# Performance work log

Measured on AMD Instinct MI355X. Metric: run time of the kernel, lower is better.

The kernel has to match this reference:

```python
import jax, jax.numpy as jnp
import numpy as np
import math

B, S, D = 2, 4096, 2048
H, HD = 16, 128          # num_heads, head_dim
W = 128                  # chunk width == stride (from/to identical)
NC = S // W              # number of chunks
ROPE_BASE = 10000.0


def _rope_tables(width, dim):
    # LlamaRotaryEmbedding: positions restart at 0 within each chunk
    inv_freq = 1.0 / (ROPE_BASE ** (jnp.arange(0, dim, 2, dtype=jnp.float32) / dim))
    t = jnp.arange(width, dtype=jnp.float32)
    freqs = jnp.outer(t, inv_freq)                 # [W, HD/2]
    emb = jnp.concatenate([freqs, freqs], axis=-1)  # [W, HD]
    return jnp.cos(emb), jnp.sin(emb)


def _rotate_half(x):
    x1, x2 = x[..., : x.shape[-1] // 2], x[..., x.shape[-1] // 2:]
    return jnp.concatenate([-x2, x1], axis=-1)


def setup_inputs() -> dict:
    key = jax.random.key(0)
    ks = jax.random.split(key, 5)
    scale = 1.0 / math.sqrt(D)
    return {
        "hidden_states": jax.random.normal(ks[0], (B, S, D), dtype=jnp.float32),
        "attention_mask": jnp.zeros((B, 1, S, S), dtype=jnp.float32),
        "wq": jax.random.normal(ks[1], (D, D), dtype=jnp.float32) * scale,
        "wk": jax.random.normal(ks[2], (D, D), dtype=jnp.float32) * scale,
        "wv": jax.random.normal(ks[3], (D, D), dtype=jnp.float32) * scale,
        "wo": jax.random.normal(ks[4], (D, D), dtype=jnp.float32) * scale,
    }


def reference(hidden_states, attention_mask, wq, wk, wv, wo):
    dtype = hidden_states.dtype
    # fold sequence into [B, NC, W, D] chunks (stride == width, S % W == 0)
    x = hidden_states.reshape(B, NC, W, D)

    def proj(w):  # torch Linear: x @ w.T ; -> [B, NC, H, W, HD]
        y = jnp.einsum("bcwd,ed->bcwe", x, w)
        return y.reshape(B, NC, W, H, HD).transpose(0, 1, 3, 2, 4)

    q, k, v = proj(wq), proj(wk), proj(wv)

    cos, sin = _rope_tables(W, HD)              # [W, HD], positions 0..W-1 per chunk
    cos = cos.astype(dtype)[None, None, None]
    sin = sin.astype(dtype)[None, None, None]
    q = q * cos + _rotate_half(q) * sin
    k = k * cos + _rotate_half(k) * sin

    scores = jnp.einsum("bchqd,bchkd->bchqk", q, k) / math.sqrt(HD)  # [B,NC,H,W,W]

    # block-diagonal slices of dense mask: [B,1,S,S] -> [B,NC,1,W,W]
    m = attention_mask.reshape(B, 1, NC, W, NC, W)
    diag = jnp.arange(NC)
    m = m[:, :, diag, :, diag, :]               # [NC, B, 1, W, W]
    m = jnp.transpose(m, (1, 0, 2, 3, 4))       # [B, NC, 1, W, W]

    scores = scores + m
    scores = jnp.maximum(scores, jnp.finfo(scores.dtype).min)
    probs = jax.nn.softmax(scores.astype(jnp.float32), axis=-1).astype(dtype)

    out = jnp.einsum("bchqk,bchkd->bchqd", probs, v)   # [B,NC,H,W,HD]
    out = out.transpose(0, 1, 3, 2, 4).reshape(B, S, D)
    return jnp.einsum("bsd,ed->bse", out, wo)
```

## Files before the change

### kernel.cpp

```cpp
#include <hip/hip_runtime.h>

typedef __bf16 bf16;
typedef __attribute__((ext_vector_type(8))) __bf16 bf16x8;
typedef __attribute__((ext_vector_type(4))) float f32x4;

#define S_LEN 4096
#define D_DIM 2048
#define LDP 136
#define BKP 40

__device__ __forceinline__ void async_cp16(const void* g, void* l) {
  __builtin_amdgcn_global_load_lds(
      (__attribute__((address_space(1))) void*)(void*)g,
      (__attribute__((address_space(3))) void*)l, 16, 0, 0);
}

__device__ __forceinline__ bf16x8 load8(const void* p, int isbf, size_t idx) {
  if (isbf) return *(const bf16x8*)((const bf16*)p + idx);
  const float* f = (const float*)p + idx;
  f32x4 a = *(const f32x4*)f;
  f32x4 b = *(const f32x4*)(f + 4);
  bf16x8 r;
  r[0] = (bf16)a[0]; r[1] = (bf16)a[1]; r[2] = (bf16)a[2]; r[3] = (bf16)a[3];
  r[4] = (bf16)b[0]; r[5] = (bf16)b[1]; r[6] = (bf16)b[2]; r[7] = (bf16)b[3];
  return r;
}
__device__ __forceinline__ float maskAt(const void* p, int isbf, size_t idx) {
  return isbf ? (float)((const bf16*)p)[idx] : ((const float*)p)[idx];
}

__global__ void sniff_kernel(const void* x, int* flag) {
  __shared__ int cnt;
  if (threadIdx.x == 0) cnt = 0;
  __syncthreads();
  const unsigned short* u = (const unsigned short*)x;
  int c = 0;
  for (int i = threadIdx.x; i < 4096; i += 256) {
    int e = (u[i] >> 7) & 0xFF;
    if (e >= 100 && e <= 141) c++;
  }
  atomicAdd(&cnt, c);
  __syncthreads();
  if (threadIdx.x == 0) *flag = (cnt >= 3500) ? 1 : 0;
}

__global__ void fill_one_kernel(unsigned int* __restrict__ o, int nwords) {
  int i = blockIdx.x * 256 + threadIdx.x;
  if (i < nwords) o[i] = 0x3F803F80u;
}

__global__ void rope_tables_kernel(bf16* __restrict__ cs, bf16* __restrict__ sn) {
  int i = blockIdx.x * 256 + threadIdx.x;
  int pos = i >> 7;
  int col = i & 127;
  int k = col & 63;
  float inv = expf(-((float)(2 * k) / 128.0f) * 9.210340371976184f);
  float f = (float)pos * inv;
  cs[i] = (bf16)cosf(f);
  sn[i] = (bf16)sinf(f);
}

__global__ __launch_bounds__(256) void convert_kernel(
    const void* __restrict__ x,  const void* __restrict__ wq,
    const void* __restrict__ wk, const void* __restrict__ wv,
    const void* __restrict__ wo,
    bf16* __restrict__ xb,  bf16* __restrict__ wqb, bf16* __restrict__ wkb,
    bf16* __restrict__ wvb, bf16* __restrict__ wob,
    const int* __restrict__ dflag) {
  const int isbf = *dflag;
  size_t g = (size_t)blockIdx.x * 256 + threadIdx.x;
  const size_t XG = 2097152u, WG = 524288u;
  const void* src; bf16* dst; size_t off;
  if (g < XG) { src = x; dst = xb; off = g; }
  else {
    size_t r = g - XG;
    int w = (int)(r >> 19);
    off = r & (WG - 1);
    src = (w == 0) ? wq : (w == 1) ? wk : (w == 2) ? wv : wo;
    dst = (w == 0) ? wqb : (w == 1) ? wkb : (w == 2) ? wvb : wob;
  }
  size_t e = off * 8;
  if (isbf) {
    *(bf16x8*)(dst + e) = *(const bf16x8*)((const bf16*)src + e);
  } else {
    const float* f = (const float*)src + e;
    f32x4 a = *(const f32x4*)f;
    f32x4 b = *(const f32x4*)(f + 4);
    bf16x8 r8;
    r8[0] = (bf16)a[0]; r8[1] = (bf16)a[1]; r8[2] = (bf16)a[2]; r8[3] = (bf16)a[3];
    r8[4] = (bf16)b[0]; r8[5] = (bf16)b[1]; r8[6] = (bf16)b[2]; r8[7] = (bf16)b[3];
    *(bf16x8*)(dst + e) = r8;
  }
}

template <bool TILED_A>
__device__ __forceinline__ void gemm_async_core(
    const bf16* __restrict__ A, const bf16* __restrict__ Bw,
    bf16* __restrict__ Cbf, float* __restrict__ Cfp, int ldc,
    int m0, int n0, int K) {
  __shared__ bf16 As[128 * 32];
  __shared__ bf16 Bs[128 * 32];
  const int tid  = threadIdx.x;
  const int lane = tid & 63;
  const int wv   = tid >> 6;
  const int wm   = (wv >> 1) * 64;
  const int wn   = (wv & 1) * 64;

  const int srow = lane >> 2;
  const int sgrp = lane & 3;
  const bf16* gA0 = A + (size_t)(m0 + wv * 32 + srow) * K + sgrp * 8;
  const bf16* gB  = Bw + (size_t)(n0 + wv * 32 + srow) * K + sgrp * 8;
  bf16* lA0 = As + (wv * 32) * 32;
  bf16* lA1 = As + (wv * 32 + 16) * 32;
  bf16* lB0 = Bs + (wv * 32) * 32;
  bf16* lB1 = Bs + (wv * 32 + 16) * 32;

  const f32x4 z4 = {0.f, 0.f, 0.f, 0.f};
  f32x4 acc[4][4];
#pragma unroll
  for (int i = 0; i < 4; i++)
#pragma unroll
    for (int j = 0; j < 4; j++) acc[i][j] = z4;

  const int fr = lane & 15;
  const int fq = lane >> 4;

  for (int k0 = 0; k0 < K; k0 += 32) {
    const bf16* gA;
    size_t astride;
    if (TILED_A) {
      gA = A + (size_t)((m0 >> 7) * 16 + (k0 >> 7)) * (128 * 128)
             + (size_t)(wv * 32 + srow) * 128 + (k0 & 127) + sgrp * 8;
      astride = 128;
    } else {
      gA = gA0 + k0;
      astride = (size_t)K;
    }
    async_cp16(gA,                 lA0);
    async_cp16(gA + 16 * astride,  lA1);
    async_cp16(gB,                 lB0);
    async_cp16(gB + (size_t)16 * K, lB1);
    gB += 32;
    __syncthreads();

    bf16x8 af[4], bfr[4];
#pragma unroll
    for (int i = 0; i < 4; i++)
      af[i] = *(const bf16x8*)(As + (wm + i * 16 + fr) * 32 + fq * 8);
#pragma unroll
    for (int j = 0; j < 4; j++)
      bfr[j] = *(const bf16x8*)(Bs + (wn + j * 16 + fr) * 32 + fq * 8);
#pragma unroll
    for (int i = 0; i < 4; i++)
#pragma unroll
      for (int j = 0; j < 4; j++)
        acc[i][j] = __builtin_amdgcn_mfma_f32_16x16x32_bf16(af[i], bfr[j], acc[i][j], 0, 0, 0);
    __syncthreads();
  }

#pragma unroll
  for (int i = 0; i < 4; i++) {
    int row = wm + i * 16 + fq * 4;
#pragma unroll
    for (int j = 0; j < 4; j++) {
      int col = wn + j * 16 + fr;
      f32x4 v = acc[i][j];
#pragma unroll
      for (int r = 0; r < 4; r++) {
        size_t off = (size_t)(row + r) * ldc + col;
        if (Cbf) Cbf[off] = (bf16)v[r];
        else     Cfp[off] = v[r];
      }
    }
  }
}

__global__ __launch_bounds__(256) void qkv_fast_kernel(
    const bf16* __restrict__ xb, const bf16* __restrict__ wqb,
    const bf16* __restrict__ wkb, const bf16* __restrict__ wvb,
    bf16* __restrict__ qb, bf16* __restrict__ kb, bf16* __restrict__ vb) {
  const int nb = blockIdx.x, mb = blockIdx.y, z = blockIdx.z;
  const bf16* Wz = (z == 0) ? wqb : (z == 1) ? wkb : wvb;
  bf16* ob = (z == 0) ? qb : (z == 1) ? kb : vb;
  bf16* Cb = ob + (size_t)(mb * 16 + nb) * (128 * 128);
  gemm_async_core<false>(xb, Wz, Cb, nullptr, 128, mb * 128, nb * 128, D_DIM);
}

__global__ __launch_bounds__(256) void oproj_fast_kernel(
    const bf16* __restrict__ aot, const bf16* __restrict__ wob,
    void* __restrict__ out, const int* __restrict__ dflag) {
  const int isbf = *dflag;
  const int nb = blockIdx.x, mb = blockIdx.y;
  size_t off = (size_t)mb * 128 * D_DIM + nb * 128;
  if (isbf)
    gemm_async_core<true>(aot, wob, (bf16*)out + off, nullptr, D_DIM, mb * 128, nb * 128, D_DIM);
  else
    gemm_async_core<true>(aot, wob, nullptr, (float*)out + off, D_DIM, mb * 128, nb * 128, D_DIM);
}

template <bool TILED_A>
__device__ __forceinline__ void gemm_bt_core(
    const void* __restrict__ A, int a_isbf,
    const void* __restrict__ Bw, int b_isbf,
    void* __restrict__ Cb, int c_isbf, int ldc, int m0, int n0, int K) {
  __shared__ bf16 As[128 * BKP];
  __shared__ bf16 Bs[128 * BKP];
  const int tid  = threadIdx.x;
  const int lane = tid & 63;
  const int wv   = tid >> 6;
  const int wm   = (wv >> 1) * 64;
  const int wn   = (wv & 1) * 64;
  const int srow = tid >> 1;
  const int shalf = tid & 1;

  const f32x4 z4 = {0.f, 0.f, 0.f, 0.f};
  f32x4 acc[4][4];
#pragma unroll
  for (int i = 0; i < 4; i++)
#pragma unroll
    for (int j = 0; j < 4; j++) acc[i][j] = z4;

  const int fr = lane & 15;
  const int fq = lane >> 4;

  for (int k0 = 0; k0 < K; k0 += 32) {
    bf16x8 a0, a1, b0, b1;
    if (TILED_A) {
      const bf16* At = (const bf16*)A
          + (size_t)((m0 >> 7) * 16 + (k0 >> 7)) * (128 * 128)
          + (size_t)srow * 128 + (k0 & 127) + shalf * 16;
      a0 = *(const bf16x8*)(At);
      a1 = *(const bf16x8*)(At + 8);
    } else {
      size_t ab = (size_t)(m0 + srow) * K + k0 + shalf * 16;
      a0 = load8(A, a_isbf, ab);
      a1 = load8(A, a_isbf, ab + 8);
    }
    {
      size_t bb = (size_t)(n0 + srow) * K + k0 + shalf * 16;
      b0 = load8(Bw, b_isbf, bb);
      b1 = load8(Bw, b_isbf, bb + 8);
    }
    __syncthreads();
    *(bf16x8*)(As + srow * BKP + shalf * 16)     = a0;
    *(bf16x8*)(As + srow * BKP + shalf * 16 + 8) = a1;
    *(bf16x8*)(Bs + srow * BKP + shalf * 16)     = b0;
    *(bf16x8*)(Bs + srow * BKP + shalf * 16 + 8) = b1;
    __syncthreads();

    bf16x8 af[4], bfr[4];
#pragma unroll
    for (int i = 0; i < 4; i++)
      af[i] = *(const bf16x8*)(As + (wm + i * 16 + fr) * BKP + fq * 8);
#pragma unroll
    for (int j = 0; j < 4; j++)
      bfr[j] = *(const bf16x8*)(Bs + (wn + j * 16 + fr) * BKP + fq * 8);
#pragma unroll
    for (int i = 0; i < 4; i++)
#pragma unroll
      for (int j = 0; j < 4; j++)
        acc[i][j] = __builtin_amdgcn_mfma_f32_16x16x32_bf16(af[i], bfr[j], acc[i][j], 0, 0, 0);
  }
#pragma unroll
  for (int i = 0; i < 4; i++) {
    int row = wm + i * 16 + fq * 4;
#pragma unroll
    for (int j = 0; j < 4; j++) {
      int col = wn + j * 16 + fr;
      f32x4 v = acc[i][j];
#pragma unroll
      for (int r = 0; r < 4; r++) {
        size_t off = (size_t)(row + r) * ldc + col;
        if (c_isbf) ((bf16*)Cb)[off] = (bf16)v[r];
        else        ((float*)Cb)[off] = v[r];
      }
    }
  }
}

__global__ __launch_bounds__(256) void qkv_kernel(
    const void* __restrict__ x, const void* __restrict__ wq,
    const void* __restrict__ wk, const void* __restrict__ wvp,
    bf16* __restrict__ qb, bf16* __restrict__ kb, bf16* __restrict__ vb,
    const int* __restrict__ dflag) {
  const int isbf = *dflag;
  const int nb = blockIdx.x, mb = blockIdx.y, z = blockIdx.z;
  const void* Wz = (z == 0) ? wq : (z == 1) ? wk : wvp;
  bf16* ob = (z == 0) ? qb : (z == 1) ? kb : vb;
  bf16* Cb = ob + (size_t)(mb * 16 + nb) * (128 * 128);
  gemm_bt_core<false>(x, isbf, Wz, isbf, Cb, 1, 128, mb * 128, nb * 128, D_DIM);
}

__global__ __launch_bounds__(256) void oproj_kernel(
    const bf16* __restrict__ aot, const void* __restrict__ wo, void* __restrict__ out,
    const int* __restrict__ dflag) {
  const int isbf = *dflag;
  const int nb = blockIdx.x, mb = blockIdx.y;
  void* Cb = isbf ? (void*)((bf16*)out + (size_t)mb * 128 * D_DIM + nb * 128)
                  : (void*)((float*)out + (size_t)mb * 128 * D_DIM + nb * 128);
  gemm_bt_core<true>(aot, 1, wo, isbf, Cb, isbf, D_DIM, mb * 128, nb * 128, D_DIM);
}

__global__ __launch_bounds__(256) void attn_kernel(
    const bf16* __restrict__ qb, const bf16* __restrict__ kb, const bf16* __restrict__ vb,
    const void* __restrict__ msk, const bf16* __restrict__ cosb, const bf16* __restrict__ sinb,
    bf16* __restrict__ qout, const int* __restrict__ dflag) {
  const int isbf = *dflag;
  const int h = blockIdx.x, c = blockIdx.y, b = blockIdx.z;
  __shared__ bf16 bufA[128 * LDP];
  __shared__ bf16 bufB[128 * LDP];
  const size_t tile = (size_t)((b * 32 + c) * 16 + h) * (128 * 128);
  const bf16* Q  = qb + tile;
  const bf16* Kt = kb + tile;
  const bf16* V  = vb + tile;
  const int tid = threadIdx.x;
  const int lane = tid & 63;
  const int wv = tid >> 6;
  const int fr = lane & 15, fq = lane >> 4;

  {
    const int row = tid >> 1;
    const int half = tid & 1;
#pragma unroll
    for (int j = 0; j < 8; j++) {
      const int g = half * 8 + j;
      const int c0 = g * 8;
      const float sgn = (c0 < 64) ? -1.f : 1.f;
      bf16x8 cv = *(const bf16x8*)(cosb + row * 128 + c0);
      bf16x8 sv = *(const bf16x8*)(sinb + row * 128 + c0);
      bf16x8 xq = *(const bf16x8*)(Q  + row * 128 + c0);
      bf16x8 pq = *(const bf16x8*)(Q  + row * 128 + (c0 ^ 64));
      bf16x8 xk = *(const bf16x8*)(Kt + row * 128 + c0);
      bf16x8 pk = *(const bf16x8*)(Kt + row * 128 + (c0 ^ 64));
      bf16x8 oq, ok;
#pragma unroll
      for (int e = 0; e < 8; e++) {
        float cf = (float)cv[e], sf = (float)sv[e];
        oq[e] = (bf16)((float)xq[e] * cf + sgn * (float)pq[e] * sf);
        ok[e] = (bf16)((float)xk[e] * cf + sgn * (float)pk[e] * sf);
      }
      *(bf16x8*)(bufA + row * LDP + c0) = oq;
      *(bf16x8*)(bufB + row * LDP + c0) = ok;
    }
  }
  __syncthreads();

  const f32x4 z4 = {0.f, 0.f, 0.f, 0.f};
  f32x4 acc[2][8];
#pragma unroll
  for (int rt = 0; rt < 2; rt++)
#pragma unroll
    for (int ct = 0; ct < 8; ct++) acc[rt][ct] = z4;

#pragma unroll
  for (int ks = 0; ks < 4; ks++) {
    bf16x8 af[2], bfr[8];
#pragma unroll
    for (int rt = 0; rt < 2; rt++)
      af[rt] = *(const bf16x8*)(bufA + (wv * 32 + rt * 16 + fr) * LDP + (ks * 4 + fq) * 8);
#pragma unroll
    for (int ct = 0; ct < 8; ct++)
      bfr[ct] = *(const bf16x8*)(bufB + (ct * 16 + fr) * LDP + (ks * 4 + fq) * 8);
#pragma unroll
    for (int rt = 0; rt < 2; rt++)
#pragma unroll
      for (int ct = 0; ct < 8; ct++)
        acc[rt][ct] = __builtin_amdgcn_mfma_f32_16x16x32_bf16(af[rt], bfr[ct], acc[rt][ct], 0, 0, 0);
  }

  const float scale = 0.08838834764831845f;
#pragma unroll
  for (int rt = 0; rt < 2; rt++) {
#pragma unroll
    for (int r = 0; r < 4; r++) {
      const int R = wv * 32 + rt * 16 + fq * 4 + r;
      const size_t mbase = ((size_t)b * S_LEN + c * 128 + R) * S_LEN + c * 128;
      float t[8];
      float mx = -3.4e38f;
#pragma unroll
      for (int ct = 0; ct < 8; ct++) {
        float s = acc[rt][ct][r] * scale + maskAt(msk, isbf, mbase + ct * 16 + fr);
        s = fmaxf(s, -3.3895313892515355e38f);
        t[ct] = s;
        mx = fmaxf(mx, s);
      }
#pragma unroll
      for (int o = 1; o < 16; o <<= 1) mx = fmaxf(mx, __shfl_xor(mx, o, 64));
      float sum = 0.f;
#pragma unroll
      for (int ct = 0; ct < 8; ct++) { float e = __expf(t[ct] - mx); t[ct] = e; sum += e; }
#pragma unroll
      for (int o = 1; o < 16; o <<= 1) sum += __shfl_xor(sum, o, 64);
      const float inv = 1.0f / sum;
#pragma unroll
      for (int ct = 0; ct < 8; ct++) acc[rt][ct][r] = t[ct] * inv;
    }
  }
  __syncthreads();

#pragma unroll
  for (int rt = 0; rt < 2; rt++)
#pragma unroll
    for (int ct = 0; ct < 8; ct++)
#pragma unroll
      for (int r = 0; r < 4; r++) {
        const int R = wv * 32 + rt * 16 + fq * 4 + r;
        const int col = ct * 16 + fr;
        bufA[R * LDP + col] = (bf16)acc[rt][ct][r];
      }
  {
    const int kw = tid >> 1;
    const int half = tid & 1;
#pragma unroll
    for (int j = 0; j < 8; j++) {
      const int c0 = half * 64 + j * 8;
      bf16x8 vvv = *(const bf16x8*)(V + kw * 128 + c0);
#pragma unroll
      for (int e = 0; e < 8; e++)
        bufB[(c0 + e) * LDP + kw] = vvv[e];
    }
  }
  __syncthreads();

  f32x4 oacc[2][8];
#pragma unroll
  for (int rt = 0; rt < 2; rt++)
#pragma unroll
    for (int ct = 0; ct < 8; ct++) oacc[rt][ct] = z4;
#pragma unroll
  for (int ks = 0; ks < 4; ks++) {
    bf16x8 af[2], bfr[8];
#pragma unroll
    for (int rt = 0; rt < 2; rt++)
      af[rt] = *(const bf16x8*)(bufA + (wv * 32 + rt * 16 + fr) * LDP + (ks * 4 + fq) * 8);
#pragma unroll
    for (int ct = 0; ct < 8; ct++)
      bfr[ct] = *(const bf16x8*)(bufB + (ct * 16 + fr) * LDP + (ks * 4 + fq) * 8);
#pragma unroll
    for (int rt = 0; rt < 2; rt++)
#pragma unroll
      for (int ct = 0; ct < 8; ct++)
        oacc[rt][ct] = __builtin_amdgcn_mfma_f32_16x16x32_bf16(af[rt], bfr[ct], oacc[rt][ct], 0, 0, 0);
  }

  bf16* ob = qout + tile;
#pragma unroll
  for (int rt = 0; rt < 2; rt++)
#pragma unroll
    for (int ct = 0; ct < 8; ct++) {
      f32x4 v = oacc[rt][ct];
#pragma unroll
      for (int r = 0; r < 4; r++) {
        const int R = wv * 32 + rt * 16 + fq * 4 + r;
        const int col = ct * 16 + fr;
        ob[(size_t)R * 128 + col] = (bf16)v[r];
      }
    }
}

extern "C" void kernel_launch(void* const* d_in, const int* in_sizes, int n_in,
                              void* d_out, int out_size, void* d_ws, size_t ws_size,
                              hipStream_t stream) {
  const void* x   = d_in[0];
  const void* msk = d_in[1];
  const void* wq  = d_in[2];
  const void* wk  = d_in[3];
  const void* wvp = d_in[4];
  const void* wo  = d_in[5];

  const size_t TSZ = (size_t)2 * S_LEN * D_DIM * sizeof(bf16);
  const size_t WSZ = (size_t)D_DIM * D_DIM * sizeof(bf16);
  const size_t need_fast = 4 * TSZ + 4 * WSZ + 65536 + 4096;
  const size_t need_safe = 3 * TSZ + 65536 + 4096;

  char* ws = (char*)d_ws;

  if (ws_size >= need_fast) {
    bf16* qb  = (bf16*)(ws);
    bf16* kb  = (bf16*)(ws + TSZ);
    bf16* vb  = (bf16*)(ws + 2 * TSZ);
    bf16* xb  = (bf16*)(ws + 3 * TSZ);
    bf16* wqb = (bf16*)(ws + 4 * TSZ);
    bf16* wkb = (bf16*)(ws + 4 * TSZ + WSZ);
    bf16* wvb = (bf16*)(ws + 4 * TSZ + 2 * WSZ);
    bf16* wob = (bf16*)(ws + 4 * TSZ + 3 * WSZ);
    bf16* cs  = (bf16*)(ws + 4 * TSZ + 4 * WSZ);
    bf16* sn  = (bf16*)(ws + 4 * TSZ + 4 * WSZ + 32768);
    int* dflag = (int*)(ws + 4 * TSZ + 4 * WSZ + 65536);

    sniff_kernel<<<dim3(1), 256, 0, stream>>>(x, dflag);
    rope_tables_kernel<<<dim3(64), 256, 0, stream>>>(cs, sn);
    convert_kernel<<<dim3(16384), 256, 0, stream>>>(x, wq, wk, wvp, wo,
                                                    xb, wqb, wkb, wvb, wob, dflag);
    qkv_fast_kernel<<<dim3(16, 64, 3), 256, 0, stream>>>(xb, wqb, wkb, wvb, qb, kb, vb);
    attn_kernel<<<dim3(16, 32, 2), 256, 0, stream>>>(qb, kb, vb, msk, cs, sn, qb, dflag);
    oproj_fast_kernel<<<dim3(16, 64), 256, 0, stream>>>(qb, wob, d_out, dflag);
  } else if (ws_size >= need_safe) {
    bf16* qb = (bf16*)(ws);
    bf16* kb = (bf16*)(ws + TSZ);
    bf16* vb = (bf16*)(ws + 2 * TSZ);
    bf16* cs = (bf16*)(ws + 3 * TSZ);
    bf16* sn = (bf16*)(ws + 3 * TSZ + 32768);
    int* dflag = (int*)(ws + 3 * TSZ + 65536);

    sniff_kernel<<<dim3(1), 256, 0, stream>>>(x, dflag);
    rope_tables_kernel<<<dim3(64), 256, 0, stream>>>(cs, sn);
    qkv_kernel<<<dim3(16, 64, 3), 256, 0, stream>>>(x, wq, wk, wvp, qb, kb, vb, dflag);
    attn_kernel<<<dim3(16, 32, 2), 256, 0, stream>>>(qb, kb, vb, msk, cs, sn, qb, dflag);
    oproj_kernel<<<dim3(16, 64), 256, 0, stream>>>(qb, wo, d_out, dflag);
  } else {
    int nwords = out_size / 2;
    fill_one_kernel<<<dim3((nwords + 255) / 256), 256, 0, stream>>>((unsigned int*)d_out, nwords);
  }
}
```

Before: 656.2 us.

## Use 32x32x16 MFMA in async GEMM core and 512-thread attention blocks

```diff
diff --git a/kernel.cpp b/kernel.cpp
--- a/kernel.cpp
+++ b/kernel.cpp
@@ -3,6 +3,7 @@
 typedef __bf16 bf16;
 typedef __attribute__((ext_vector_type(8))) __bf16 bf16x8;
 typedef __attribute__((ext_vector_type(4))) float f32x4;
+typedef __attribute__((ext_vector_type(16))) float f32x16;
 
 #define S_LEN 4096
 #define D_DIM 2048
@@ -115,15 +116,16 @@
   bf16* lB0 = Bs + (wv * 32) * 32;
   bf16* lB1 = Bs + (wv * 32 + 16) * 32;
 
-  const f32x4 z4 = {0.f, 0.f, 0.f, 0.f};
-  f32x4 acc[4][4];
-#pragma unroll
-  for (int i = 0; i < 4; i++)
-#pragma unroll
-    for (int j = 0; j < 4; j++) acc[i][j] = z4;
-
-  const int fr = lane & 15;
-  const int fq = lane >> 4;
+  f32x16 acc[2][2];
+#pragma unroll
+  for (int i = 0; i < 2; i++)
+#pragma unroll
+    for (int j = 0; j < 2; j++)
+#pragma unroll
+      for (int e = 0; e < 16; e++) acc[i][j][e] = 0.f;
+
+  const int fl = lane & 31;
+  const int kh = lane >> 5;
 
   for (int k0 = 0; k0 < K; k0 += 32) {
     const bf16* gA;
@@ -143,36 +145,42 @@
     gB += 32;
     __syncthreads();
 
-    bf16x8 af[4], bfr[4];
-#pragma unroll
-    for (int i = 0; i < 4; i++)
-      af[i] = *(const bf16x8*)(As + (wm + i * 16 + fr) * 32 + fq * 8);
-#pragma unroll
-    for (int j = 0; j < 4; j++)
-      bfr[j] = *(const bf16x8*)(Bs + (wn + j * 16 + fr) * 32 + fq * 8);
-#pragma unroll
-    for (int i = 0; i < 4; i++)
-#pragma unroll
-      for (int j = 0; j < 4; j++)
-        acc[i][j] = __builtin_amdgcn_mfma_f32_16x16x32_bf16(af[i], bfr[j], acc[i][j], 0, 0, 0);
+    bf16x8 af[2][2], bfr[2][2];
+#pragma unroll
+    for (int i = 0; i < 2; i++)
+#pragma unroll
+      for (int kk = 0; kk < 2; kk++)
+        af[i][kk] = *(const bf16x8*)(As + (wm + i * 32 + fl) * 32 + kk * 16 + kh * 8);
+#pragma unroll
+    for (int j = 0; j < 2; j++)
+#pragma unroll
+      for (int kk = 0; kk < 2; kk++)
+        bfr[j][kk] = *(const bf16x8*)(Bs + (wn + j * 32 + fl) * 32 + kk * 16 + kh * 8);
+#pragma unroll
+    for (int i = 0; i < 2; i++)
+#pragma unroll
+      for (int j = 0; j < 2; j++)
+#pragma unroll
+        for (int kk = 0; kk < 2; kk++)
+          acc[i][j] = __builtin_amdgcn_mfma_f32_32x32x16_bf16(
+              af[i][kk], bfr[j][kk], acc[i][j], 0, 0, 0);
     __syncthreads();
   }
 
 #pragma unroll
-  for (int i = 0; i < 4; i++) {
-    int row = wm + i * 16 + fq * 4;
-#pragma unroll
-    for (int j = 0; j < 4; j++) {
-      int col = wn + j * 16 + fr;
-      f32x4 v = acc[i][j];
-#pragma unroll
-      for (int r = 0; r < 4; r++) {
-        size_t off = (size_t)(row + r) * ldc + col;
+  for (int i = 0; i < 2; i++)
+#pragma unroll
+    for (int j = 0; j < 2; j++) {
+      f32x16 v = acc[i][j];
+      const int col = wn + j * 32 + fl;
+#pragma unroll
+      for (int r = 0; r < 16; r++) {
+        const int row = wm + i * 32 + (r & 3) + 8 * (r >> 2) + 4 * kh;
+        size_t off = (size_t)row * ldc + col;
         if (Cbf) Cbf[off] = (bf16)v[r];
         else     Cfp[off] = v[r];
       }
     }
-  }
 }
 
 __global__ __launch_bounds__(256) void qkv_fast_kernel(
@@ -301,7 +309,7 @@
   gemm_bt_core<true>(aot, 1, wo, isbf, Cb, isbf, D_DIM, mb * 128, nb * 128, D_DIM);
 }
 
-__global__ __launch_bounds__(256) void attn_kernel(
+__global__ __launch_bounds__(512) void attn_kernel(
     const bf16* __restrict__ qb, const bf16* __restrict__ kb, const bf16* __restrict__ vb,
     const void* __restrict__ msk, const bf16* __restrict__ cosb, const bf16* __restrict__ sinb,
     bf16* __restrict__ qout, const int* __restrict__ dflag) {
@@ -319,12 +327,11 @@
   const int fr = lane & 15, fq = lane >> 4;
 
   {
-    const int row = tid >> 1;
-    const int half = tid & 1;
-#pragma unroll
-    for (int j = 0; j < 8; j++) {
-      const int g = half * 8 + j;
-      const int c0 = g * 8;
+    const int row = tid >> 2;
+    const int q4 = tid & 3;
+#pragma unroll
+    for (int j = 0; j < 4; j++) {
+      const int c0 = q4 * 32 + j * 8;
       const float sgn = (c0 < 64) ? -1.f : 1.f;
       bf16x8 cv = *(const bf16x8*)(cosb + row * 128 + c0);
       bf16x8 sv = *(const bf16x8*)(sinb + row * 128 + c0);
@@ -346,74 +353,62 @@
   __syncthreads();
 
   const f32x4 z4 = {0.f, 0.f, 0.f, 0.f};
-  f32x4 acc[2][8];
-#pragma unroll
-  for (int rt = 0; rt < 2; rt++)
-#pragma unroll
-    for (int ct = 0; ct < 8; ct++) acc[rt][ct] = z4;
+  f32x4 acc[8];
+#pragma unroll
+  for (int ct = 0; ct < 8; ct++) acc[ct] = z4;
 
 #pragma unroll
   for (int ks = 0; ks < 4; ks++) {
-    bf16x8 af[2], bfr[8];
-#pragma unroll
-    for (int rt = 0; rt < 2; rt++)
-      af[rt] = *(const bf16x8*)(bufA + (wv * 32 + rt * 16 + fr) * LDP + (ks * 4 + fq) * 8);
+    bf16x8 af = *(const bf16x8*)(bufA + (wv * 16 + fr) * LDP + (ks * 4 + fq) * 8);
+    bf16x8 bfr[8];
 #pragma unroll
     for (int ct = 0; ct < 8; ct++)
       bfr[ct] = *(const bf16x8*)(bufB + (ct * 16 + fr) * LDP + (ks * 4 + fq) * 8);
 #pragma unroll
-    for (int rt = 0; rt < 2; rt++)
-#pragma unroll
-      for (int ct = 0; ct < 8; ct++)
-        acc[rt][ct] = __builtin_amdgcn_mfma_f32_16x16x32_bf16(af[rt], bfr[ct], acc[rt][ct], 0, 0, 0);
+    for (int ct = 0; ct < 8; ct++)
+      acc[ct] = __builtin_amdgcn_mfma_f32_16x16x32_bf16(af, bfr[ct], acc[ct], 0, 0, 0);
   }
 
   const float scale = 0.08838834764831845f;
 #pragma unroll
-  for (int rt = 0; rt < 2; rt++) {
+  for (int r = 0; r < 4; r++) {
+    const int R = wv * 16 + fq * 4 + r;
+    const size_t mbase = ((size_t)b * S_LEN + c * 128 + R) * S_LEN + c * 128;
+    float t[8];
+    float mx = -3.4e38f;
+#pragma unroll
+    for (int ct = 0; ct < 8; ct++) {
+      float s = acc[ct][r] * scale + maskAt(msk, isbf, mbase + ct * 16 + fr);
+      s = fmaxf(s, -3.3895313892515355e38f);
+      t[ct] = s;
+      mx = fmaxf(mx, s);
+    }
+#pragma unroll
+    for (int o = 1; o < 16; o <<= 1) mx = fmaxf(mx, __shfl_xor(mx, o, 64));
+    float sum = 0.f;
+#pragma unroll
+    for (int ct = 0; ct < 8; ct++) { float e = __expf(t[ct] - mx); t[ct] = e; sum += e; }
+#pragma unroll
+    for (int o = 1; o < 16; o <<= 1) sum += __shfl_xor(sum, o, 64);
+    const float inv = 1.0f / sum;
+#pragma unroll
+    for (int ct = 0; ct < 8; ct++) acc[ct][r] = t[ct] * inv;
+  }
+  __syncthreads();
+
+#pragma unroll
+  for (int ct = 0; ct < 8; ct++)
 #pragma unroll
     for (int r = 0; r < 4; r++) {
-      const int R = wv * 32 + rt * 16 + fq * 4 + r;
-      const size_t mbase = ((size_t)b * S_LEN + c * 128 + R) * S_LEN + c * 128;
-      float t[8];
-      float mx = -3.4e38f;
-#pragma unroll
-      for (int ct = 0; ct < 8; ct++) {
-        float s = acc[rt][ct][r] * scale + maskAt(msk, isbf, mbase + ct * 16 + fr);
-        s = fmaxf(s, -3.3895313892515355e38f);
-        t[ct] = s;
-        mx = fmaxf(mx, s);
-      }
-#pragma unroll
-      for (int o = 1; o < 16; o <<= 1) mx = fmaxf(mx, __shfl_xor(mx, o, 64));
-      float sum = 0.f;
-#pragma unroll
-      for (int ct = 0; ct < 8; ct++) { float e = __expf(t[ct] - mx); t[ct] = e; sum += e; }
-#pragma unroll
-      for (int o = 1; o < 16; o <<= 1) sum += __shfl_xor(sum, o, 64);
-      const float inv = 1.0f / sum;
-#pragma unroll
-      for (int ct = 0; ct < 8; ct++) acc[rt][ct][r] = t[ct] * inv;
-    }
-  }
-  __syncthreads();
-
-#pragma unroll
-  for (int rt = 0; rt < 2; rt++)
-#pragma unroll
-    for (int ct = 0; ct < 8; ct++)
-#pragma unroll
-      for (int r = 0; r < 4; r++) {
-        const int R = wv * 32 + rt * 16 + fq * 4 + r;
-        const int col = ct * 16 + fr;
-        bufA[R * LDP + col] = (bf16)acc[rt][ct][r];
-      }
+      const int R = wv * 16 + fq * 4 + r;
+      bufA[R * LDP + ct * 16 + fr] = (bf16)acc[ct][r];
+    }
   {
-    const int kw = tid >> 1;
-    const int half = tid & 1;
-#pragma unroll
-    for (int j = 0; j < 8; j++) {
-      const int c0 = half * 64 + j * 8;
+    const int kw = tid >> 2;
+    const int q4 = tid & 3;
+#pragma unroll
+    for (int j = 0; j < 4; j++) {
+      const int c0 = q4 * 32 + j * 8;
       bf16x8 vvv = *(const bf16x8*)(V + kw * 128 + c0);
 #pragma unroll
       for (int e = 0; e < 8; e++)
@@ -422,40 +417,32 @@
   }
   __syncthreads();
 
-  f32x4 oacc[2][8];
-#pragma unroll
-  for (int rt = 0; rt < 2; rt++)
-#pragma unroll
-    for (int ct = 0; ct < 8; ct++) oacc[rt][ct] = z4;
+  f32x4 oacc[8];
+#pragma unroll
+  for (int ct = 0; ct < 8; ct++) oacc[ct] = z4;
 #pragma unroll
   for (int ks = 0; ks < 4; ks++) {
-    bf16x8 af[2], bfr[8];
-#pragma unroll
-    for (int rt = 0; rt < 2; rt++)
-      af[rt] = *(const bf16x8*)(bufA + (wv * 32 + rt * 16 + fr) * LDP + (ks * 4 + fq) * 8);
+    bf16x8 af = *(const bf16x8*)(bufA + (wv * 16 + fr) * LDP + (ks * 4 + fq) * 8);
+    bf16x8 bfr[8];
 #pragma unroll
     for (int ct = 0; ct < 8; ct++)
       bfr[ct] = *(const bf16x8*)(bufB + (ct * 16 + fr) * LDP + (ks * 4 + fq) * 8);
 #pragma unroll
-    for (int rt = 0; rt < 2; rt++)
-#pragma unroll
-      for (int ct = 0; ct < 8; ct++)
-        oacc[rt][ct] = __builtin_amdgcn_mfma_f32_16x16x32_bf16(af[rt], bfr[ct], oacc[rt][ct], 0, 0, 0);
+    for (int ct = 0; ct < 8; ct++)
+      oacc[ct] = __builtin_amdgcn_mfma_f32_16x16x32_bf16(af, bfr[ct], oacc[ct], 0, 0, 0);
   }
 
   bf16* ob = qout + tile;
 #pragma unroll
-  for (int rt = 0; rt < 2; rt++)
-#pragma unroll
-    for (int ct = 0; ct < 8; ct++) {
-      f32x4 v = oacc[rt][ct];
-#pragma unroll
-      for (int r = 0; r < 4; r++) {
-        const int R = wv * 32 + rt * 16 + fq * 4 + r;
-        const int col = ct * 16 + fr;
-        ob[(size_t)R * 128 + col] = (bf16)v[r];
-      }
-    }
+  for (int ct = 0; ct < 8; ct++) {
+    f32x4 v = oacc[ct];
+#pragma unroll
+    for (int r = 0; r < 4; r++) {
+      const int R = wv * 16 + fq * 4 + r;
+      const int col = ct * 16 + fr;
+      ob[(size_t)R * 128 + col] = (bf16)v[r];
+    }
+  }
 }
 
 extern "C" void kernel_launch(void* const* d_in, const int* in_sizes, int n_in,
@@ -493,7 +480,7 @@
     convert_kernel<<<dim3(16384), 256, 0, stream>>>(x, wq, wk, wvp, wo,
                                                     xb, wqb, wkb, wvb, wob, dflag);
     qkv_fast_kernel<<<dim3(16, 64, 3), 256, 0, stream>>>(xb, wqb, wkb, wvb, qb, kb, vb);
-    attn_kernel<<<dim3(16, 32, 2), 256, 0, stream>>>(qb, kb, vb, msk, cs, sn, qb, dflag);
+    attn_kernel<<<dim3(16, 32, 2), 512, 0, stream>>>(qb, kb, vb, msk, cs, sn, qb, dflag);
     oproj_fast_kernel<<<dim3(16, 64), 256, 0, stream>>>(qb, wob, d_out, dflag);
   } else if (ws_size >= need_safe) {
     bf16* qb = (bf16*)(ws);
@@ -506,7 +493,7 @@
     sniff_kernel<<<dim3(1), 256, 0, stream>>>(x, dflag);
     rope_tables_kernel<<<dim3(64), 256, 0, stream>>>(cs, sn);
     qkv_kernel<<<dim3(16, 64, 3), 256, 0, stream>>>(x, wq, wk, wvp, qb, kb, vb, dflag);
-    attn_kernel<<<dim3(16, 32, 2), 256, 0, stream>>>(qb, kb, vb, msk, cs, sn, qb, dflag);
+    attn_kernel<<<dim3(16, 32, 2), 512, 0, stream>>>(qb, kb, vb, msk, cs, sn, qb, dflag);
     oproj_kernel<<<dim3(16, 64), 256, 0, stream>>>(qb, wo, d_out, dflag);
   } else {
     int nwords = out_size / 2;
```

Result: slower. 685.5 us (+4.5%).
